# Performance work log

Measured on AMD Instinct MI355X. Metric: run time of the kernel, lower is better.

Reference implementation:

```python
import jax, jax.numpy as jnp
import numpy as np

N = 10000      # nodes
E = 320000     # edges
F_IN = 33      # input node features
H = 32         # hidden
G = 64         # graphs in batch


def setup_inputs() -> dict:
    key = jax.random.key(0)
    ks = jax.random.split(key, 24)
    s = 0.1  # small init scale for numerical sanity
    inp = {
        "x": jax.random.normal(ks[0], (N, F_IN), jnp.float32),
        "edge_index": jax.random.randint(ks[1], (2, E), 0, N, jnp.int32),
        "edge_attr": jax.random.uniform(ks[2], (E, 1), jnp.float32),
        "batch": jnp.sort(jax.random.randint(ks[3], (N,), 0, G, jnp.int32)),
        # conv1: edge-MLP Linear(1 -> F_IN*H), root weight [F_IN,H], bias [H]
        "nn_w1": jax.random.normal(ks[4], (1, F_IN * H), jnp.float32) * s,
        "nn_b1": jax.random.normal(ks[5], (F_IN * H,), jnp.float32) * s,
        "root1": jax.random.normal(ks[6], (F_IN, H), jnp.float32) * s,
        "bias1": jnp.zeros((H,), jnp.float32),
        # conv2: edge-MLP Linear(1 -> H*H)
        "nn_w2": jax.random.normal(ks[7], (1, H * H), jnp.float32) * s,
        "nn_b2": jax.random.normal(ks[8], (H * H,), jnp.float32) * s,
        "root2": jax.random.normal(ks[9], (H, H), jnp.float32) * s,
        "bias2": jnp.zeros((H,), jnp.float32),
        # conv3
        "nn_w3": jax.random.normal(ks[10], (1, H * H), jnp.float32) * s,
        "nn_b3": jax.random.normal(ks[11], (H * H,), jnp.float32) * s,
        "root3": jax.random.normal(ks[12], (H, H), jnp.float32) * s,
        "bias3": jnp.zeros((H,), jnp.float32),
        # readout MLP: Linear(3H -> H), Linear(H -> 2)
        "lin1_w": jax.random.normal(ks[13], (3 * H, H), jnp.float32) * s,
        "lin1_b": jnp.zeros((H,), jnp.float32),
        "lin2_w": jax.random.normal(ks[14], (H, 2), jnp.float32) * s,
        "lin2_b": jnp.zeros((2,), jnp.float32),
    }
    return inp


def _nnconv(x, src, dst, edge_attr, nn_w, nn_b, root, bias):
    """PyG NNConv (aggr='add'): out_i = x_i @ root + bias + sum_{e: dst(e)=i} x_{src(e)} @ Theta(e_attr)."""
    in_dim, out_dim = root.shape
    # per-edge weight matrix from edge MLP: [E, in, out]
    W = (edge_attr @ nn_w + nn_b).reshape(-1, in_dim, out_dim)
    msg = jnp.einsum('ei,eio->eo', x[src], W)          # gather + per-edge small matmul
    agg = jax.ops.segment_sum(msg, dst, num_segments=N)  # scatter-add into targets
    return agg + x @ root + bias


def reference(x, edge_index, edge_attr, batch,
              nn_w1, nn_b1, root1, bias1,
              nn_w2, nn_b2, root2, bias2,
              nn_w3, nn_b3, root3, bias3,
              lin1_w, lin1_b, lin2_w, lin2_b):
    src, dst = edge_index[0], edge_index[1]
    h = jax.nn.relu(_nnconv(x, src, dst, edge_attr, nn_w1, nn_b1, root1, bias1))
    h = jax.nn.relu(_nnconv(h, src, dst, edge_attr, nn_w2, nn_b2, root2, bias2))
    h = jax.nn.relu(_nnconv(h, src, dst, edge_attr, nn_w3, nn_b3, root3, bias3))
    # global add / mean / max pooling over graphs
    add_p = jax.ops.segment_sum(h, batch, num_segments=G)
    cnt = jax.ops.segment_sum(jnp.ones((N, 1), h.dtype), batch, num_segments=G)
    mean_p = add_p / jnp.maximum(cnt, 1.0)
    max_p = jax.ops.segment_max(h, batch, num_segments=G)
    max_p = jnp.where(jnp.isfinite(max_p), max_p, 0.0)  # guard empty segments
    g = jnp.concatenate([add_p, mean_p, max_p], axis=1)  # [G, 3H]
    g = jax.nn.relu(g @ lin1_w + lin1_b)
    # dropout p=0.5 is identity in eval mode
    logits = g @ lin2_w + lin2_b
    return jax.nn.log_softmax(logits, axis=-1)
```

## Files before the change

### kernel.cpp

```cpp
#include <hip/hip_runtime.h>

constexpr int N_  = 10000;
constexpr int E_  = 320000;
constexpr int F1  = 33;
constexpr int H   = 32;
constexpr int G   = 64;
constexpr int CAP = 96;
constexpr int NB_ = 1280;
constexpr int ROW = CAP * 8;

constexpr int EBLK = E_ / 256;
constexpr int PBLK = N_ / 8;
constexpr int SLICES = 32;
constexpr int CHUNKS = 32;
constexpr int TILE   = 320;
constexpr int ITERS  = TILE / 32;

__device__ __forceinline__ unsigned bf16r(float x) {
    unsigned u = __float_as_uint(x);
    return (u + 0x7FFFu + ((u >> 16) & 1u)) >> 16;
}

__device__ __forceinline__ size_t mslot(int n, int pos) {
    return (size_t)(n >> 3) * ROW + (size_t)(pos >> 3) * 64 + (n & 7) * 8 + (pos & 7);
}


__global__ __launch_bounds__(256) void k_build_pre1(
        const int* __restrict__ ei, const float* __restrict__ ea,
        const float* __restrict__ x, const int* __restrict__ batch,
        const float* __restrict__ A, const float* __restrict__ Bm,
        const float* __restrict__ Rw, const float* __restrict__ bias,
        int* __restrict__ counts, unsigned* __restrict__ meta2,
        unsigned* __restrict__ UVs, float* __restrict__ Rs,
        int* __restrict__ startsP) {
    __shared__ unsigned s_uv[32][9];
    __shared__ float    s_r[32][9];
    if (blockIdx.x < EBLK) {
        int e = blockIdx.x * 256 + threadIdx.x;
        int s = ei[e];
        int d = ei[E_ + e];
        int pos = atomicAdd(&counts[d], 1);
        meta2[mslot(d, pos)] = (unsigned)s | (bf16r(ea[e]) << 16);
    } else {
        int base8 = (blockIdx.x - EBLK) * 8;
        int grp = threadIdx.x >> 5;
        int f = threadIdx.x & 31;
        int node = base8 + grp;
        if (f == 0) {
            int b = batch[node];
            int bp = (node == 0) ? -1 : batch[node - 1];
            if (b != bp) startsP[b] = node + 1;
        }
        float u = 0.f, v = 0.f, r = bias[f];
        const float* xr = x + (size_t)node * F1;
        #pragma unroll
        for (int k = 0; k < F1; ++k) {
            float xv = xr[k];
            u = fmaf(xv, A[k * H + f], u);
            v = fmaf(xv, Bm[k * H + f], v);
            r = fmaf(xv, Rw[k * H + f], r);
        }
        s_uv[f][grp] = bf16r(u) | (bf16r(v) << 16);
        s_r[f][grp]  = r;
        __syncthreads();
        int fo = threadIdx.x >> 3;
        int nl = threadIdx.x & 7;
        UVs[(size_t)fo * N_ + base8 + nl] = s_uv[fo][nl];
        Rs [(size_t)fo * N_ + base8 + nl] = s_r [fo][nl];
    }
}


__global__ __launch_bounds__(256) void k_pre(
        const float* __restrict__ Hs,
        const float* __restrict__ A, const float* __restrict__ Bm,
        const float* __restrict__ Rw, const float* __restrict__ bias,
        unsigned* __restrict__ UVs, float* __restrict__ Rs) {
    __shared__ unsigned s_uv[32][9];
    __shared__ float    s_r[32][9];
    int base8 = blockIdx.x * 8;
    int grp = threadIdx.x >> 5;
    int f = threadIdx.x & 31;
    int node = base8 + grp;
    float hv = Hs[(size_t)f * N_ + node];
    float u = 0.f, v = 0.f, r = bias[f];
    #pragma unroll
    for (int k = 0; k < H; ++k) {
        float hk = __shfl(hv, k, 32);
        u = fmaf(hk, A[k * H + f], u);
        v = fmaf(hk, Bm[k * H + f], v);
        r = fmaf(hk, Rw[k * H + f], r);
    }
    s_uv[f][grp] = bf16r(u) | (bf16r(v) << 16);
    s_r[f][grp]  = r;
    __syncthreads();
    int fo = threadIdx.x >> 3;
    int nl = threadIdx.x & 7;
    UVs[(size_t)fo * N_ + base8 + nl] = s_uv[fo][nl];
    Rs [(size_t)fo * N_ + base8 + nl] = s_r [fo][nl];
}


__global__ __launch_bounds__(256) void k_agg_lds(
        const int* __restrict__ counts, const unsigned* __restrict__ meta2,
        const unsigned* __restrict__ UVs, const float* __restrict__ Rs,
        float* __restrict__ Hs) {
    __shared__ __align__(16) unsigned uvl[N_];
    int s     = blockIdx.x & 31;
    int chunk = blockIdx.x >> 5;

    int l   = threadIdx.x & 63;
    int wav = threadIdx.x >> 6;
    int j0  = l & 7;
    int nl  = l >> 3;

    int cbase = chunk * TILE + wav * 8;
    int node = cbase + nl;
    int nc = min(node, N_ - 1);
    int dg = (node < N_) ? counts[nc] : 0;
    float rv = Rs[(size_t)s * N_ + nc];
    const unsigned* mrow = meta2 + (size_t)(cbase >> 3) * ROW + l;
    unsigned m0 = mrow[0], m1 = mrow[64], m2 = mrow[128],
             m3 = mrow[192], m4 = mrow[256], m5 = mrow[320];

    const unsigned* srcp = UVs + (size_t)s * N_;
    #pragma unroll
    for (int i = 0; i < 10; ++i) {
        int d4 = (i * 256 + threadIdx.x) * 4;
        if (d4 + 4 <= N_) {
            uint4 t = *reinterpret_cast<const uint4*>(srcp + d4);
            *reinterpret_cast<uint4*>(&uvl[d4]) = t;
        }
    }
    __syncthreads();

    for (int it = 0; it < ITERS; ++it) {
        int nbase = cbase + 32;
        int nnode = nbase + nl;
        int nnc = min(nnode, N_ - 1);
        int ndg = 0; float nrv = 0.f;
        unsigned n0 = 0, n1 = 0, n2 = 0, n3 = 0, n4 = 0, n5 = 0;
        if (it < ITERS - 1) {
            ndg = (nnode < N_) ? counts[nnc] : 0;
            nrv = Rs[(size_t)s * N_ + nnc];
            const unsigned* nmr = meta2 + (size_t)(nbase >> 3) * ROW + l;
            n0 = nmr[0]; n1 = nmr[64]; n2 = nmr[128];
            n3 = nmr[192]; n4 = nmr[256]; n5 = nmr[320];
        }

        int maxd = dg;
        maxd = max(maxd, __shfl_xor(maxd, 8));
        maxd = max(maxd, __shfl_xor(maxd, 16));
        maxd = max(maxd, __shfl_xor(maxd, 32));
        float acc = 0.f;
        auto slot = [&](int p, unsigned mv) {
            unsigned idx = min(mv & 0xFFFFu, (unsigned)(N_ - 1));
            unsigned w = uvl[idx];
            float t = fmaf(__uint_as_float(mv & 0xFFFF0000u),
                           __uint_as_float(w << 16),
                           __uint_as_float(w & 0xFFFF0000u));
            if (j0 + 8 * p < dg) acc += t;
        };
        if (maxd > 0)  slot(0, m0);
        if (maxd > 8)  slot(1, m1);
        if (maxd > 16) slot(2, m2);
        if (maxd > 24) slot(3, m3);
        if (maxd > 32) slot(4, m4);
        if (maxd > 40) slot(5, m5);
        if (maxd > 48) {
            const unsigned* trow = meta2 + (size_t)(cbase >> 3) * ROW + l;
            for (int p = 6; 8 * p < maxd; ++p)
                slot(p, trow[p * 64]);
        }
        acc += __shfl_xor(acc, 1);
        acc += __shfl_xor(acc, 2);
        acc += __shfl_xor(acc, 4);
        float h = fmaxf(rv + acc, 0.f);
        if (j0 == 0 && node < N_) Hs[(size_t)s * N_ + node] = h;

        cbase = nbase; node = nnode; nc = nnc; dg = ndg; rv = nrv;
        m0 = n0; m1 = n1; m2 = n2; m3 = n3; m4 = n4; m5 = n5;
    }
}


__global__ __launch_bounds__(256) void k_pool(
        const float* __restrict__ Hs, const int* __restrict__ startsP,
        const float* __restrict__ w1, const float* __restrict__ b1,
        const float* __restrict__ w2, const float* __restrict__ b2,
        float* __restrict__ out) {
    __shared__ int sst[G];
    __shared__ float ga[32], gm[32], gx[32];
    int tid = threadIdx.x;
    if (tid < G) sst[tid] = startsP[tid];
    __syncthreads();
    int g = blockIdx.x;
    int sp = sst[g];
    int s = 0, e = 0;
    if (sp != 0) {
        s = sp - 1;
        e = N_;
        for (int j = g + 1; j < G; ++j)
            if (sst[j]) { e = sst[j] - 1; break; }
    }
    int f = tid >> 3, oct = tid & 7;
    float sum = 0.f, mx = 0.f;
    for (int n = s + oct; n < e; n += 8) {
        float w = Hs[(size_t)f * N_ + n];
        sum += w;
        mx = fmaxf(mx, w);
    }
    sum += __shfl_xor(sum, 1); mx = fmaxf(mx, __shfl_xor(mx, 1));
    sum += __shfl_xor(sum, 2); mx = fmaxf(mx, __shfl_xor(mx, 2));
    sum += __shfl_xor(sum, 4); mx = fmaxf(mx, __shfl_xor(mx, 4));
    if (oct == 0) {
        float c = fmaxf((float)(e - s), 1.0f);
        ga[f] = sum;
        gm[f] = sum / c;
        gx[f] = mx;
    }
    __syncthreads();
    if (tid < 32) {
        float hacc = b1[tid];
        #pragma unroll
        for (int k = 0; k < H; ++k) {
            hacc = fmaf(ga[k], w1[k * H + tid], hacc);
            hacc = fmaf(gm[k], w1[(H + k) * H + tid], hacc);
            hacc = fmaf(gx[k], w1[(2 * H + k) * H + tid], hacc);
        }
        float hid = fmaxf(hacc, 0.f);
        float p0 = hid * w2[tid * 2 + 0];
        float p1 = hid * w2[tid * 2 + 1];
        #pragma unroll
        for (int offq = 16; offq; offq >>= 1) {
            p0 += __shfl_xor(p0, offq, 32);
            p1 += __shfl_xor(p1, offq, 32);
        }
        if (tid == 0) {
            float l0 = p0 + b2[0], l1 = p1 + b2[1];
            float m = fmaxf(l0, l1);
            float lse = m + logf(expf(l0 - m) + expf(l1 - m));
            out[g * 2 + 0] = l0 - lse;
            out[g * 2 + 1] = l1 - lse;
        }
    }
}


extern "C" void kernel_launch(void* const* d_in, const int* in_sizes, int n_in,
                              void* d_out, int out_size, void* d_ws, size_t ws_size,
                              hipStream_t stream) {
    const float* x      = (const float*)d_in[0];
    const int*   ei     = (const int*)  d_in[1];
    const float* ea     = (const float*)d_in[2];
    const int*   batch  = (const int*)  d_in[3];
    const float* nn_w1  = (const float*)d_in[4];
    const float* nn_b1  = (const float*)d_in[5];
    const float* root1  = (const float*)d_in[6];
    const float* bias1  = (const float*)d_in[7];
    const float* nn_w2  = (const float*)d_in[8];
    const float* nn_b2  = (const float*)d_in[9];
    const float* root2  = (const float*)d_in[10];
    const float* bias2  = (const float*)d_in[11];
    const float* nn_w3  = (const float*)d_in[12];
    const float* nn_b3  = (const float*)d_in[13];
    const float* root3  = (const float*)d_in[14];
    const float* bias3  = (const float*)d_in[15];
    const float* lin1_w = (const float*)d_in[16];
    const float* lin1_b = (const float*)d_in[17];
    const float* lin2_w = (const float*)d_in[18];
    const float* lin2_b = (const float*)d_in[19];
    float* out = (float*)d_out;

    char* ws = (char*)d_ws;
    size_t off = 0;
    auto alloc = [&](size_t bytes) -> void* {
        void* p = ws + off;
        off += (bytes + 255) & ~(size_t)255;
        return p;
    };
    const size_t zbytes = N_ * sizeof(int) + G * sizeof(int);
    char* zchunk = (char*)alloc(zbytes);
    int*  counts  = (int*)zchunk;
    int*  startsP = (int*)(zchunk + N_ * sizeof(int));
    unsigned* meta2 = (unsigned*)alloc((size_t)NB_ * ROW * sizeof(unsigned));
    unsigned* UVs1 = (unsigned*)alloc((size_t)H * N_ * sizeof(unsigned));
    unsigned* UVs2 = (unsigned*)alloc((size_t)H * N_ * sizeof(unsigned));
    unsigned* UVs3 = (unsigned*)alloc((size_t)H * N_ * sizeof(unsigned));
    float* Rs1 = (float*)alloc((size_t)H * N_ * sizeof(float));
    float* Rs2 = (float*)alloc((size_t)H * N_ * sizeof(float));
    float* Rs3 = (float*)alloc((size_t)H * N_ * sizeof(float));
    float* h1  = (float*)alloc((size_t)H * N_ * sizeof(float));
    float* h2  = (float*)alloc((size_t)H * N_ * sizeof(float));
    float* h3  = (float*)alloc((size_t)H * N_ * sizeof(float));

    hipMemsetAsync(zchunk, 0, zbytes, stream);

    k_build_pre1<<<EBLK + PBLK, 256, 0, stream>>>(ei, ea, x, batch,
                                                  nn_w1, nn_b1, root1, bias1,
                                                  counts, meta2, UVs1, Rs1, startsP);

    k_agg_lds<<<SLICES * CHUNKS, 256, 0, stream>>>(counts, meta2, UVs1, Rs1, h1);
    k_pre    <<<PBLK, 256, 0, stream>>>(h1, nn_w2, nn_b2, root2, bias2, UVs2, Rs2);
    k_agg_lds<<<SLICES * CHUNKS, 256, 0, stream>>>(counts, meta2, UVs2, Rs2, h2);
    k_pre    <<<PBLK, 256, 0, stream>>>(h2, nn_w3, nn_b3, root3, bias3, UVs3, Rs3);
    k_agg_lds<<<SLICES * CHUNKS, 256, 0, stream>>>(counts, meta2, UVs3, Rs3, h3);

    k_pool<<<G, 256, 0, stream>>>(h3, startsP, lin1_w, lin1_b, lin2_w, lin2_b, out);
}
```

Measured before the change: 188.3 us.

## Fuse next-layer pre-transform into aggregation kernel via last-block ticket

Removes the separate k_pre launches by having the last of the 32 slice-blocks finishing each node chunk, detected with an atomic ticket counter, compute the next layer's UV/R projections for that chunk. This cuts two kernel launches and their global round-trip and launch gaps. In exchange, the projection work for each chunk runs serially in a single block at the tail of the aggregation kernel, which can add tail latency and reduce parallelism. The ticket counters are zeroed by the existing memset.

```diff
diff --git a/kernel.cpp b/kernel.cpp
--- a/kernel.cpp
+++ b/kernel.cpp
@@ -72,40 +72,15 @@
 }
 
 
-__global__ __launch_bounds__(256) void k_pre(
-        const float* __restrict__ Hs,
-        const float* __restrict__ A, const float* __restrict__ Bm,
-        const float* __restrict__ Rw, const float* __restrict__ bias,
-        unsigned* __restrict__ UVs, float* __restrict__ Rs) {
-    __shared__ unsigned s_uv[32][9];
-    __shared__ float    s_r[32][9];
-    int base8 = blockIdx.x * 8;
-    int grp = threadIdx.x >> 5;
-    int f = threadIdx.x & 31;
-    int node = base8 + grp;
-    float hv = Hs[(size_t)f * N_ + node];
-    float u = 0.f, v = 0.f, r = bias[f];
-    #pragma unroll
-    for (int k = 0; k < H; ++k) {
-        float hk = __shfl(hv, k, 32);
-        u = fmaf(hk, A[k * H + f], u);
-        v = fmaf(hk, Bm[k * H + f], v);
-        r = fmaf(hk, Rw[k * H + f], r);
-    }
-    s_uv[f][grp] = bf16r(u) | (bf16r(v) << 16);
-    s_r[f][grp]  = r;
-    __syncthreads();
-    int fo = threadIdx.x >> 3;
-    int nl = threadIdx.x & 7;
-    UVs[(size_t)fo * N_ + base8 + nl] = s_uv[fo][nl];
-    Rs [(size_t)fo * N_ + base8 + nl] = s_r [fo][nl];
-}
-
-
+template<bool DO_PRE>
 __global__ __launch_bounds__(256) void k_agg_lds(
         const int* __restrict__ counts, const unsigned* __restrict__ meta2,
         const unsigned* __restrict__ UVs, const float* __restrict__ Rs,
-        float* __restrict__ Hs) {
+        float* __restrict__ Hs,
+        const float* __restrict__ A2, const float* __restrict__ B2,
+        const float* __restrict__ Rw2, const float* __restrict__ bi2,
+        unsigned* __restrict__ UVo, float* __restrict__ Ro,
+        unsigned* __restrict__ tickets) {
     __shared__ __align__(16) unsigned uvl[N_];
     int s     = blockIdx.x & 31;
     int chunk = blockIdx.x >> 5;
@@ -181,6 +156,36 @@
 
         cbase = nbase; node = nnode; nc = nnc; dg = ndg; rv = nrv;
         m0 = n0; m1 = n1; m2 = n2; m3 = n3; m4 = n4; m5 = n5;
+    }
+
+    if (DO_PRE) {
+        __shared__ unsigned s_rank;
+        __threadfence();
+        __syncthreads();
+        if (threadIdx.x == 0)
+            s_rank = __hip_atomic_fetch_add(&tickets[chunk], 1u, __ATOMIC_ACQ_REL,
+                                            __HIP_MEMORY_SCOPE_AGENT);
+        __syncthreads();
+        if (s_rank == (unsigned)(SLICES - 1)) {
+            int grp = threadIdx.x >> 5, f = threadIdx.x & 31;
+            int cstart = chunk * TILE;
+            for (int t = 0; t < TILE / 8; ++t) {
+                int nd = cstart + t * 8 + grp;
+                if (nd < N_) {
+                    float hv = Hs[(size_t)f * N_ + nd];
+                    float u = 0.f, v = 0.f, r = bi2[f];
+                    #pragma unroll
+                    for (int k = 0; k < H; ++k) {
+                        float hk = __shfl(hv, k, 32);
+                        u = fmaf(hk, A2[k * H + f], u);
+                        v = fmaf(hk, B2[k * H + f], v);
+                        r = fmaf(hk, Rw2[k * H + f], r);
+                    }
+                    UVo[(size_t)f * N_ + nd] = bf16r(u) | (bf16r(v) << 16);
+                    Ro [(size_t)f * N_ + nd] = r;
+                }
+            }
+        }
     }
 }
 
@@ -280,10 +285,12 @@
         off += (bytes + 255) & ~(size_t)255;
         return p;
     };
-    const size_t zbytes = N_ * sizeof(int) + G * sizeof(int);
+    const size_t zbytes = N_ * sizeof(int) + G * sizeof(int) + 2 * CHUNKS * sizeof(unsigned);
     char* zchunk = (char*)alloc(zbytes);
     int*  counts  = (int*)zchunk;
     int*  startsP = (int*)(zchunk + N_ * sizeof(int));
+    unsigned* tick1 = (unsigned*)(startsP + G);
+    unsigned* tick2 = tick1 + CHUNKS;
     unsigned* meta2 = (unsigned*)alloc((size_t)NB_ * ROW * sizeof(unsigned));
     unsigned* UVs1 = (unsigned*)alloc((size_t)H * N_ * sizeof(unsigned));
     unsigned* UVs2 = (unsigned*)alloc((size_t)H * N_ * sizeof(unsigned));
@@ -301,11 +308,15 @@
                                                   nn_w1, nn_b1, root1, bias1,
                                                   counts, meta2, UVs1, Rs1, startsP);
 
-    k_agg_lds<<<SLICES * CHUNKS, 256, 0, stream>>>(counts, meta2, UVs1, Rs1, h1);
-    k_pre    <<<PBLK, 256, 0, stream>>>(h1, nn_w2, nn_b2, root2, bias2, UVs2, Rs2);
-    k_agg_lds<<<SLICES * CHUNKS, 256, 0, stream>>>(counts, meta2, UVs2, Rs2, h2);
-    k_pre    <<<PBLK, 256, 0, stream>>>(h2, nn_w3, nn_b3, root3, bias3, UVs3, Rs3);
-    k_agg_lds<<<SLICES * CHUNKS, 256, 0, stream>>>(counts, meta2, UVs3, Rs3, h3);
+    k_agg_lds<true><<<SLICES * CHUNKS, 256, 0, stream>>>(
+        counts, meta2, UVs1, Rs1, h1,
+        nn_w2, nn_b2, root2, bias2, UVs2, Rs2, tick1);
+    k_agg_lds<true><<<SLICES * CHUNKS, 256, 0, stream>>>(
+        counts, meta2, UVs2, Rs2, h2,
+        nn_w3, nn_b3, root3, bias3, UVs3, Rs3, tick2);
+    k_agg_lds<false><<<SLICES * CHUNKS, 256, 0, stream>>>(
+        counts, meta2, UVs3, Rs3, h3,
+        nullptr, nullptr, nullptr, nullptr, nullptr, nullptr, nullptr);
 
     k_pool<<<G, 256, 0, stream>>>(h3, startsP, lin1_w, lin1_b, lin2_w, lin2_b, out);
 }
```

Result: slower. 506.1 us (+168.7%).
